# Performance work log

Hardware: AMD Instinct MI355X
Metric: run time of the kernel (lower is better)

## Reference

```python
import jax, jax.numpy as jnp
import numpy as np

L2_REG = 0.02


def setup_inputs() -> dict:
    key = jax.random.key(0)
    k1, k2 = jax.random.split(key)
    n, d = 4096, 1024
    anchors = jax.random.normal(k1, (n, d), dtype=jnp.float32)
    positives = jax.random.normal(k2, (n, d), dtype=jnp.float32)
    return {"anchors": anchors, "positives": positives}


def reference(anchors, positives):
    # Fused equivalent of the per-row masked_select loop:
    # x[i, j] = a_i . (p_j - p_i) = S[i, j] - S[i, i], for j != i
    n = anchors.shape[0]
    S = anchors @ positives.T                     # (n, n)
    x = S - jnp.diag(S)[:, None]                  # subtract anchor-positive sim per row
    offdiag = ~jnp.eye(n, dtype=bool)
    # sum over negatives j != i of exp(x[i, j])
    s = jnp.sum(jnp.where(offdiag, jnp.exp(x), 0.0), axis=1)  # (n,)
    n_pair = jnp.mean(jnp.log1p(s))
    l2 = jnp.sum(anchors ** 2 + positives ** 2) / n
    return n_pair + L2_REG * l2
```

## Files before the change

### kernel.cpp

```cpp
#include <hip/hip_runtime.h>
#include <math.h>
#include <stdint.h>

#define N 4096
#define Dm 1024
#define BK 64
#define NT (Dm / BK)
#define NCB (N / 64)
#define NPART 512

typedef __attribute__((ext_vector_type(8))) short bf16x8;
typedef __attribute__((ext_vector_type(4))) float f32x4;

typedef const void __attribute__((address_space(1)))* gas_t;
typedef void __attribute__((address_space(3)))* las_t;

static __device__ __forceinline__ void gload_lds16(const void* g, void* l) {
    __builtin_amdgcn_global_load_lds((gas_t)g, (las_t)l, 16, 0, 0);
}

static __device__ __forceinline__ unsigned short f2bf(float f) {
    unsigned int u = __float_as_uint(f);
    unsigned int r = (u + 0x7fff + ((u >> 16) & 1)) >> 16;
    return (unsigned short)r;
}

__global__ __launch_bounds__(256) void prep_kernel(const float* __restrict__ A,
                                                   const float* __restrict__ P,
                                                   unsigned short* __restrict__ Abf,
                                                   unsigned short* __restrict__ Pbf,
                                                   float* __restrict__ D,
                                                   float* __restrict__ rowl2) {
    int t = threadIdx.x;
    int lane = t & 63;
    int row = blockIdx.x * 4 + (t >> 6);
    const float4* a4 = (const float4*)(A + (size_t)row * Dm);
    const float4* p4 = (const float4*)(P + (size_t)row * Dm);
    ushort4* ao = (ushort4*)(Abf + (size_t)row * Dm);
    ushort4* po = (ushort4*)(Pbf + (size_t)row * Dm);
    float dot = 0.0f, l2 = 0.0f;
#pragma unroll
    for (int c = 0; c < 4; ++c) {
        int idx = c * 64 + lane;
        float4 a = a4[idx], p = p4[idx];
        ushort4 ab, pb;
        ab.x = f2bf(a.x); ab.y = f2bf(a.y); ab.z = f2bf(a.z); ab.w = f2bf(a.w);
        pb.x = f2bf(p.x); pb.y = f2bf(p.y); pb.z = f2bf(p.z); pb.w = f2bf(p.w);
        ao[idx] = ab; po[idx] = pb;
        dot += a.x * p.x + a.y * p.y + a.z * p.z + a.w * p.w;
        l2  += a.x * a.x + a.y * a.y + a.z * a.z + a.w * a.w
             + p.x * p.x + p.y * p.y + p.z * p.z + p.w * p.w;
    }
#pragma unroll
    for (int off = 32; off; off >>= 1) {
        dot += __shfl_xor(dot, off, 64);
        l2  += __shfl_xor(l2,  off, 64);
    }
    if (lane == 0) {
        D[row]     = dot;
        rowl2[row] = l2;
    }
}

#define STAGE_TILE(gp, lp, kt) do {                                            \
        gload_lds16((gp) + (kt),                    (lp)         + tid * 8);   \
        gload_lds16((gp) + (kt) +  64 * (size_t)Dm, (lp) + 4096  + tid * 8);   \
        gload_lds16((gp) + (kt) + 128 * (size_t)Dm, (lp) + 8192  + tid * 8);   \
        gload_lds16((gp) + (kt) + 192 * (size_t)Dm, (lp) + 12288 + tid * 8);   \
    } while (0)

#define STAGE_B_HALF(lpB, kt, h) do {                                          \
        gload_lds16(gB + (kt) + ((h) ? 128 * (size_t)Dm : (size_t)0),          \
                    (lpB) + (h) * 8192 + tid * 8);                             \
        gload_lds16(gB + (kt) + ((h) ? 192 * (size_t)Dm : 64 * (size_t)Dm),    \
                    (lpB) + (h) * 8192 + 4096 + tid * 8);                      \
    } while (0)

#define DO_MFMA(I, AK0, AK1)                                                   \
    _Pragma("unroll")                                                          \
    for (int j = 0; j < 4; ++j)                                                \
        acc[I][j] = __builtin_amdgcn_mfma_f32_16x16x32_bf16(AK0, bfrag[j][0], acc[I][j], 0, 0, 0); \
    _Pragma("unroll")                                                          \
    for (int j = 0; j < 4; ++j)                                                \
        acc[I][j] = __builtin_amdgcn_mfma_f32_16x16x32_bf16(AK1, bfrag[j][1], acc[I][j], 0, 0, 0);

#define PHASE_BODY(P, STAGE_STMT, TAIL)                                        \
    {                                                                          \
        bf16x8 a0k0 = *(const bf16x8*)(aT + (2*(P))     * 16 * BK + aoff0);    \
        bf16x8 a0k1 = *(const bf16x8*)(aT + (2*(P))     * 16 * BK + aoff1);    \
        bf16x8 a1k0 = *(const bf16x8*)(aT + (2*(P) + 1) * 16 * BK + aoff0);    \
        bf16x8 a1k1 = *(const bf16x8*)(aT + (2*(P) + 1) * 16 * BK + aoff1);    \
        STAGE_STMT;                                                            \
        __builtin_amdgcn_s_barrier();                                          \
        asm volatile("s_waitcnt lgkmcnt(0)" ::: "memory");                     \
        __builtin_amdgcn_sched_barrier(0);                                     \
        __builtin_amdgcn_s_setprio(1);                                         \
        DO_MFMA(2*(P),     a0k0, a0k1)                                         \
        DO_MFMA(2*(P) + 1, a1k0, a1k1)                                         \
        __builtin_amdgcn_s_setprio(0);                                         \
        TAIL;                                                                  \
    }

__global__ __launch_bounds__(512, 2) void npair_mfma(const unsigned short* __restrict__ Abf,
                                                     const unsigned short* __restrict__ Pbf,
                                                     const float* __restrict__ D,
                                                     float* __restrict__ Mpart,
                                                     float* __restrict__ Spart) {
    __shared__ unsigned short As[2][256 * BK];
    __shared__ unsigned short Bs[2][256 * BK];

    int tid = threadIdx.x;
    int lane = tid & 63;
    int wid = tid >> 6;
    int wr = wid >> 2, wc = wid & 3;

    int bid = blockIdx.y * gridDim.x + blockIdx.x;
    int xcd = bid & 7, lid = bid >> 3;
    int by = (xcd >> 1) * 4 + (lid >> 3);
    int bx = (xcd & 1) * 8 + (lid & 7);
    int row0 = by * 256, col0 = bx * 256;

    int srow = tid >> 3;
    int kcol = (tid & 7) ^ (srow & 7);
    const unsigned short* gA = Abf + (size_t)(row0 + srow) * Dm + (kcol << 3);
    const unsigned short* gB = Pbf + (size_t)(col0 + srow) * Dm + (kcol << 3);

    STAGE_TILE(gA, &As[0][0], 0);
    STAGE_TILE(gB, &Bs[0][0], 0);
    STAGE_TILE(gA, &As[1][0], BK);
    STAGE_TILE(gB, &Bs[1][0], BK);
    asm volatile("s_waitcnt vmcnt(8)" ::: "memory");
    __builtin_amdgcn_s_barrier();

    int l15 = lane & 15;
    int aoff0 = (((lane >> 4)    ) ^ (lane & 7)) << 3;
    int aoff1 = (((lane >> 4) + 4) ^ (lane & 7)) << 3;
    const unsigned short* aBase = &As[0][0] + (wr * 128 + l15) * BK;
    const unsigned short* bBase = &Bs[0][0] + (wc * 64  + l15) * BK;

    f32x4 acc[8][4] = {};
    bf16x8 bfrag[4][2];

#pragma unroll 2
    for (int t = 0; t < NT; ++t) {
        const unsigned short* aT = aBase + (t & 1) * (256 * BK);
        const unsigned short* bT = bBase + (t & 1) * (256 * BK);
        unsigned short* stA = &As[(t + 1) & 1][0];
        unsigned short* stB = &Bs[t & 1][0];

#pragma unroll
        for (int j = 0; j < 4; ++j) {
            bfrag[j][0] = *(const bf16x8*)(bT + j * 16 * BK + aoff0);
            bfrag[j][1] = *(const bf16x8*)(bT + j * 16 * BK + aoff1);
        }
        PHASE_BODY(0,
            { if (t >= 1 && t + 1 < NT) STAGE_TILE(gA, stA, (t + 1) * BK); },
            __builtin_amdgcn_s_barrier())
        PHASE_BODY(1,
            { if (t + 2 < NT) STAGE_B_HALF(stB, (t + 2) * BK, 0); },
            __builtin_amdgcn_s_barrier())
        PHASE_BODY(2,
            { if (t + 2 < NT) STAGE_B_HALF(stB, (t + 2) * BK, 1); },
            __builtin_amdgcn_s_barrier())
        PHASE_BODY(3,
            { },
            {
                if (t < NT - 2)       { asm volatile("s_waitcnt vmcnt(4)" ::: "memory"); }
                else if (t == NT - 2) { asm volatile("s_waitcnt vmcnt(0)" ::: "memory"); }
                if (t < NT - 1) __builtin_amdgcn_s_barrier();
            })
    }

    __builtin_amdgcn_sched_barrier(0);

    int cb = bx * 4 + wc;
#pragma unroll
    for (int i = 0; i < 8; ++i) {
        int rloc = wr * 128 + i * 16 + ((lane >> 4) << 2);
#pragma unroll
        for (int e = 0; e < 4; ++e) {
            int gr = row0 + rloc + e;
            float Dv = D[gr];
            float xs[4];
            float m = -INFINITY;
#pragma unroll
            for (int j = 0; j < 4; ++j) {
                int gc = col0 + wc * 64 + j * 16 + (lane & 15);
                float x = acc[i][j][e] - Dv;
                if (gr == gc) x = -INFINITY;
                xs[j] = x;
                m = fmaxf(m, x);
            }
#pragma unroll
            for (int off = 8; off; off >>= 1) m = fmaxf(m, __shfl_xor(m, off, 64));
            float s = 0.0f;
#pragma unroll
            for (int j = 0; j < 4; ++j) s += __expf(xs[j] - m);
#pragma unroll
            for (int off = 8; off; off >>= 1) s += __shfl_xor(s, off, 64);
            if ((lane & 15) == 0) {
                Mpart[(size_t)gr * NCB + cb] = m;
                Spart[(size_t)gr * NCB + cb] = s;
            }
        }
    }
}

__global__ __launch_bounds__(256) void combine_rows(const float* __restrict__ Mpart,
                                                    const float* __restrict__ Spart,
                                                    const float* __restrict__ rowl2,
                                                    float* __restrict__ partL,
                                                    float* __restrict__ partR) {
    int t = threadIdx.x;
    int lane = t & 63;
    int w = t >> 6;
    __shared__ float ls[8];
#pragma unroll
    for (int r = 0; r < 2; ++r) {
        int row = blockIdx.x * 8 + w * 2 + r;
        float mp = Mpart[(size_t)row * NCB + lane];
        float sp = Spart[(size_t)row * NCB + lane];
        float m = mp;
#pragma unroll
        for (int off = 32; off; off >>= 1) m = fmaxf(m, __shfl_xor(m, off, 64));
        float s = sp * __expf(mp - m);
#pragma unroll
        for (int off = 32; off; off >>= 1) s += __shfl_xor(s, off, 64);
        if (lane == 0) ls[w * 2 + r] = m + logf(__expf(-m) + s);
    }
    __syncthreads();
    if (t == 0) {
        int r8 = blockIdx.x * 8;
        float L = 0.0f, R = 0.0f;
#pragma unroll
        for (int r = 0; r < 8; ++r) { L += ls[r]; R += rowl2[r8 + r]; }
        partL[blockIdx.x] = L;
        partR[blockIdx.x] = R;
    }
}

__global__ __launch_bounds__(256) void final_reduce(const float* __restrict__ partL,
                                                    const float* __restrict__ partR,
                                                    float* __restrict__ out) {
    int t = threadIdx.x;
    float accL = partL[t] + partL[t + 256];
    float acc2 = partR[t] + partR[t + 256];
#pragma unroll
    for (int off = 32; off; off >>= 1) {
        accL += __shfl_xor(accL, off, 64);
        acc2 += __shfl_xor(acc2, off, 64);
    }
    __shared__ float sa[4], sb[4];
    int wave = t >> 6;
    if ((t & 63) == 0) { sa[wave] = accL; sb[wave] = acc2; }
    __syncthreads();
    if (t == 0) {
        float L  = sa[0] + sa[1] + sa[2] + sa[3];
        float l2 = sb[0] + sb[1] + sb[2] + sb[3];
        out[0] = L / (float)N + 0.02f * (l2 / (float)N);
    }
}

extern "C" void kernel_launch(void* const* d_in, const int* in_sizes, int n_in,
                              void* d_out, int out_size, void* d_ws, size_t ws_size,
                              hipStream_t stream) {
    const float* A = (const float*)d_in[0];
    const float* P = (const float*)d_in[1];
    float* out = (float*)d_out;

    unsigned short* Abf = (unsigned short*)d_ws;
    unsigned short* Pbf = Abf + (size_t)N * Dm;
    float* D     = (float*)(Pbf + (size_t)N * Dm);
    float* rowl2 = D + N;
    float* partL = rowl2 + N;
    float* partR = partL + NPART;
    float* Mpart = partR + NPART;
    float* Spart = Mpart + (size_t)N * NCB;

    prep_kernel<<<N / 4, 256, 0, stream>>>(A, P, Abf, Pbf, D, rowl2);
    dim3 grid(16, 16);
    npair_mfma<<<grid, 512, 0, stream>>>(Abf, Pbf, D, Mpart, Spart);
    combine_rows<<<N / 8, 256, 0, stream>>>(Mpart, Spart, rowl2, partL, partR);
    final_reduce<<<1, 256, 0, stream>>>(partL, partR, out);
}
```

Measured before the change: 123.6 us.

## Software-pipeline LDS fragment reads across MFMA phases with double-buffered registers

Restructures the GEMM main loop so the A and B fragment reads from LDS for the next phase (and the next tile) are issued before the current phase's MFMAs. It removes the explicit lgkmcnt(0) wait before each MFMA block. Register-level double buffering of the A and B fragments lets LDS latency hide behind matrix math. The cost is more VGPR pressure from the doubled fragment buffers, and the ordering of barriers and waits must stay correct.

```diff
diff --git a/kernel.cpp b/kernel.cpp
--- a/kernel.cpp
+++ b/kernel.cpp
@@ -76,30 +76,84 @@
                     (lpB) + (h) * 8192 + 4096 + tid * 8);                      \
     } while (0)
 
-#define DO_MFMA(I, AK0, AK1)                                                   \
+#define READ_A4(dst, buf, rg0) do {                                            \
+        dst[0] = *(const bf16x8*)((buf) + ((rg0)     * 16) * BK + aoff0);      \
+        dst[1] = *(const bf16x8*)((buf) + ((rg0)     * 16) * BK + aoff1);      \
+        dst[2] = *(const bf16x8*)((buf) + ((rg0) + 1) * 16 * BK + aoff0);      \
+        dst[3] = *(const bf16x8*)((buf) + ((rg0) + 1) * 16 * BK + aoff1);      \
+    } while (0)
+
+#define READ_B8(PAR, buf) do {                                                 \
+        _Pragma("unroll")                                                      \
+        for (int j = 0; j < 4; ++j) {                                          \
+            bfr[PAR][j][0] = *(const bf16x8*)((buf) + j * 16 * BK + aoff0);    \
+            bfr[PAR][j][1] = *(const bf16x8*)((buf) + j * 16 * BK + aoff1);    \
+        }                                                                      \
+    } while (0)
+
+#define MFMA_PH(P, ap, BP)                                                     \
     _Pragma("unroll")                                                          \
     for (int j = 0; j < 4; ++j)                                                \
-        acc[I][j] = __builtin_amdgcn_mfma_f32_16x16x32_bf16(AK0, bfrag[j][0], acc[I][j], 0, 0, 0); \
+        acc[2*(P)][j]   = __builtin_amdgcn_mfma_f32_16x16x32_bf16(ap[0], bfr[BP][j][0], acc[2*(P)][j],   0, 0, 0); \
     _Pragma("unroll")                                                          \
     for (int j = 0; j < 4; ++j)                                                \
-        acc[I][j] = __builtin_amdgcn_mfma_f32_16x16x32_bf16(AK1, bfrag[j][1], acc[I][j], 0, 0, 0);
-
-#define PHASE_BODY(P, STAGE_STMT, TAIL)                                        \
-    {                                                                          \
-        bf16x8 a0k0 = *(const bf16x8*)(aT + (2*(P))     * 16 * BK + aoff0);    \
-        bf16x8 a0k1 = *(const bf16x8*)(aT + (2*(P))     * 16 * BK + aoff1);    \
-        bf16x8 a1k0 = *(const bf16x8*)(aT + (2*(P) + 1) * 16 * BK + aoff0);    \
-        bf16x8 a1k1 = *(const bf16x8*)(aT + (2*(P) + 1) * 16 * BK + aoff1);    \
-        STAGE_STMT;                                                            \
+        acc[2*(P)][j]   = __builtin_amdgcn_mfma_f32_16x16x32_bf16(ap[1], bfr[BP][j][1], acc[2*(P)][j],   0, 0, 0); \
+    _Pragma("unroll")                                                          \
+    for (int j = 0; j < 4; ++j)                                                \
+        acc[2*(P)+1][j] = __builtin_amdgcn_mfma_f32_16x16x32_bf16(ap[2], bfr[BP][j][0], acc[2*(P)+1][j], 0, 0, 0); \
+    _Pragma("unroll")                                                          \
+    for (int j = 0; j < 4; ++j)                                                \
+        acc[2*(P)+1][j] = __builtin_amdgcn_mfma_f32_16x16x32_bf16(ap[3], bfr[BP][j][1], acc[2*(P)+1][j], 0, 0, 0);
+
+#define TILE_BODY(CUR, NXT) do {                                               \
+        const unsigned short* aT  = aBase + (CUR) * 16384;                     \
+        const unsigned short* aTn = aBase + (NXT) * 16384;                     \
+        const unsigned short* bTn = bBase + (NXT) * 16384;                     \
+        unsigned short* stA = &As[NXT][0];                                     \
+        unsigned short* stB = &Bs[CUR][0];                                     \
+         \
+        READ_A4(aF[1], aT, 2);                                                 \
+        if (t >= 1 && t <= 14) STAGE_TILE(gA, stA, (t + 1) * BK);              \
+        __builtin_amdgcn_sched_barrier(0);                                     \
+        __builtin_amdgcn_s_setprio(1);                                         \
+        MFMA_PH(0, aF[0], CUR)                                                 \
+        __builtin_amdgcn_s_setprio(0);                                         \
+        __builtin_amdgcn_sched_barrier(0);                                     \
         __builtin_amdgcn_s_barrier();                                          \
-        asm volatile("s_waitcnt lgkmcnt(0)" ::: "memory");                     \
+         \
+        READ_A4(aF[0], aT, 4);                                                 \
+        if (t <= 13) STAGE_B_HALF(stB, (t + 2) * BK, 0);                       \
         __builtin_amdgcn_sched_barrier(0);                                     \
         __builtin_amdgcn_s_setprio(1);                                         \
-        DO_MFMA(2*(P),     a0k0, a0k1)                                         \
-        DO_MFMA(2*(P) + 1, a1k0, a1k1)                                         \
+        MFMA_PH(1, aF[1], CUR)                                                 \
         __builtin_amdgcn_s_setprio(0);                                         \
-        TAIL;                                                                  \
-    }
+        __builtin_amdgcn_sched_barrier(0);                                     \
+        __builtin_amdgcn_s_barrier();                                          \
+         \
+        READ_A4(aF[1], aT, 6);                                                 \
+        if (t <= 13) STAGE_B_HALF(stB, (t + 2) * BK, 1);                       \
+        __builtin_amdgcn_sched_barrier(0);                                     \
+        __builtin_amdgcn_s_setprio(1);                                         \
+        MFMA_PH(2, aF[0], CUR)                                                 \
+        __builtin_amdgcn_s_setprio(0);                                         \
+        __builtin_amdgcn_sched_barrier(0);                                     \
+        __builtin_amdgcn_s_barrier();                                          \
+           \
+        if (t <= 13)      { asm volatile("s_waitcnt vmcnt(4)" ::: "memory"); } \
+        else if (t == 14) { asm volatile("s_waitcnt vmcnt(0)" ::: "memory"); } \
+        if (t <= 14) {                                                         \
+            __builtin_amdgcn_s_barrier();                                      \
+            __builtin_amdgcn_sched_barrier(0);                                 \
+            READ_B8(NXT, bTn);                                                 \
+            READ_A4(aF[0], aTn, 0);                                            \
+        }                                                                      \
+        __builtin_amdgcn_sched_barrier(0);                                     \
+        __builtin_amdgcn_s_setprio(1);                                         \
+        MFMA_PH(3, aF[1], CUR)                                                 \
+        __builtin_amdgcn_s_setprio(0);                                         \
+        __builtin_amdgcn_sched_barrier(0);                                     \
+        if (t <= 13) __builtin_amdgcn_s_barrier();                             \
+    } while (0)
 
 __global__ __launch_bounds__(512, 2) void npair_mfma(const unsigned short* __restrict__ Abf,
                                                      const unsigned short* __restrict__ Pbf,
@@ -131,6 +185,7 @@
     STAGE_TILE(gB, &Bs[1][0], BK);
     asm volatile("s_waitcnt vmcnt(8)" ::: "memory");
     __builtin_amdgcn_s_barrier();
+    __builtin_amdgcn_sched_barrier(0);
 
     int l15 = lane & 15;
     int aoff0 = (((lane >> 4)    ) ^ (lane & 7)) << 3;
@@ -139,36 +194,17 @@
     const unsigned short* bBase = &Bs[0][0] + (wc * 64  + l15) * BK;
 
     f32x4 acc[8][4] = {};
-    bf16x8 bfrag[4][2];
-
-#pragma unroll 2
-    for (int t = 0; t < NT; ++t) {
-        const unsigned short* aT = aBase + (t & 1) * (256 * BK);
-        const unsigned short* bT = bBase + (t & 1) * (256 * BK);
-        unsigned short* stA = &As[(t + 1) & 1][0];
-        unsigned short* stB = &Bs[t & 1][0];
-
-#pragma unroll
-        for (int j = 0; j < 4; ++j) {
-            bfrag[j][0] = *(const bf16x8*)(bT + j * 16 * BK + aoff0);
-            bfrag[j][1] = *(const bf16x8*)(bT + j * 16 * BK + aoff1);
-        }
-        PHASE_BODY(0,
-            { if (t >= 1 && t + 1 < NT) STAGE_TILE(gA, stA, (t + 1) * BK); },
-            __builtin_amdgcn_s_barrier())
-        PHASE_BODY(1,
-            { if (t + 2 < NT) STAGE_B_HALF(stB, (t + 2) * BK, 0); },
-            __builtin_amdgcn_s_barrier())
-        PHASE_BODY(2,
-            { if (t + 2 < NT) STAGE_B_HALF(stB, (t + 2) * BK, 1); },
-            __builtin_amdgcn_s_barrier())
-        PHASE_BODY(3,
-            { },
-            {
-                if (t < NT - 2)       { asm volatile("s_waitcnt vmcnt(4)" ::: "memory"); }
-                else if (t == NT - 2) { asm volatile("s_waitcnt vmcnt(0)" ::: "memory"); }
-                if (t < NT - 1) __builtin_amdgcn_s_barrier();
-            })
+    bf16x8 bfr[2][4][2];
+    bf16x8 aF[2][4];
+
+    READ_B8(0, bBase);
+    READ_A4(aF[0], aBase, 0);
+
+    for (int tt = 0; tt < NT / 2; ++tt) {
+        int t = 2 * tt;
+        TILE_BODY(0, 1);
+        t = 2 * tt + 1;
+        TILE_BODY(1, 0);
     }
 
     __builtin_amdgcn_sched_barrier(0);
```

After: 122.3 us. No clear change (-1.1%).
